# Kernel optimization log

Hardware: AMD Instinct MI355X
Metric: run time of the kernel (lower is better)

Reference implementation:

```python
import jax, jax.numpy as jnp
import numpy as np

B, S, D = 4, 4096, 2048
R_SSM = 6                      # ar_ssm_max_rank hardcoded in block
R_FFN = max(D // 96, 4)        # UltraLowRankFFN rank = 21
EPS = 1e-6


def rmsnorm(x, w):
    rms = jnp.sqrt(jnp.mean(x * x, axis=-1, keepdims=True) + EPS)
    return w * (x / rms)


def setup_inputs() -> dict:
    key = jax.random.key(0)
    ks = jax.random.split(key, 8)
    x = jax.random.normal(ks[0], (B, S, D), dtype=jnp.float32)
    norm1_w = jnp.ones((D,), dtype=jnp.float32)
    norm2_w = jnp.ones((D,), dtype=jnp.float32)
    # low-rank semiseparable AR-SSM params: in-proj U, decays lam, out-proj V
    U = jax.random.normal(ks[1], (D, R_SSM), dtype=jnp.float32) / np.sqrt(D)
    lam = jax.random.normal(ks[2], (R_SSM,), dtype=jnp.float32)
    V = jax.random.normal(ks[3], (R_SSM, D), dtype=jnp.float32) / np.sqrt(R_SSM)
    # ultra low-rank FFN
    W1 = jax.random.normal(ks[4], (D, R_FFN), dtype=jnp.float32) / np.sqrt(D)
    W2 = jax.random.normal(ks[5], (R_FFN, D), dtype=jnp.float32) / np.sqrt(R_FFN)
    return {"x": x, "norm1_w": norm1_w, "U": U, "lam": lam, "V": V,
            "norm2_w": norm2_w, "W1": W1, "W2": W2}


def reference(x, norm1_w, U, lam, V, norm2_w, W1, W2):
    # --- sublayer 1: RMSNorm -> low-rank semiseparable AR-SSM scan -> residual ---
    xn = rmsnorm(x, norm1_w)                     # [B,S,D]
    u = jnp.einsum('bsd,dr->bsr', xn, U)         # [B,S,r] low-rank input proj
    a = jax.nn.sigmoid(lam)                      # [r] stable decays in (0,1)

    def step(h, u_t):
        h = a * h + u_t                          # h: [B,r]
        return h, h

    h0 = jnp.zeros((B, R_SSM), dtype=x.dtype)
    _, hs = jax.lax.scan(step, h0, jnp.swapaxes(u, 0, 1))  # hs: [S,B,r]
    y = jnp.einsum('sbr,rd->bsd', hs, V)         # out proj back to d_model
    x = x + y

    # --- sublayer 2: RMSNorm -> ultra low-rank FFN (d->r->d, GELU) -> residual ---
    xn2 = rmsnorm(x, norm2_w)
    ffn = jnp.einsum('bsr,rd->bsd', jax.nn.gelu(jnp.einsum('bsd,dr->bsr', xn2, W1)), W2)
    return x + ffn
```

## Files before the change

kernel.cpp:

```cpp
#include <hip/hip_runtime.h>
#include <math.h>

namespace {
constexpr int S_ = 4096, D_ = 2048;
constexpr int RS_ = 6, RF_ = 21;
constexpr float EPS_ = 1e-6f;

typedef float floatx4 __attribute__((ext_vector_type(4)));

#define DPP_ADD_(v, ctrl) \
  v += __int_as_float(__builtin_amdgcn_update_dpp(0, __float_as_int(v), ctrl, 0xF, 0xF, true))

__device__ __forceinline__ float wave_sum(float v) {
  DPP_ADD_(v, 0x111);
  DPP_ADD_(v, 0x112);
  DPP_ADD_(v, 0x114);
  DPP_ADD_(v, 0x118);
  DPP_ADD_(v, 0x142);
  DPP_ADD_(v, 0x143);
  return __int_as_float(__builtin_amdgcn_readlane(__float_as_int(v), 63));
}

__device__ __forceinline__ float rdlane(float v, int l) {
  return __int_as_float(__builtin_amdgcn_readlane(__float_as_int(v), l));
}

__device__ __forceinline__ float sel_lane(float old, float val, int tgt, int lane) {
  return (lane == tgt) ? val : old;
}

__device__ __forceinline__ float gelu_f(float x) {
  float i2 = 1.5957691216057308f * fmaf(0.044715f * x * x, x, x);
  return x * __builtin_amdgcn_rcpf(1.f + __expf(-i2));
}

__device__ __forceinline__ float dot4(float4 a, float4 b) {
  return fmaf(a.x, b.x, fmaf(a.y, b.y, fmaf(a.z, b.z, a.w * b.w)));
}

__device__ __forceinline__ float4 fma4(float s, float4 a, float4 c) {
  return make_float4(fmaf(s, a.x, c.x), fmaf(s, a.y, c.y), fmaf(s, a.z, c.z),
                     fmaf(s, a.w, c.w));
}

__device__ __forceinline__ void ld4(float4 (&q)[4], const float* p) {
  q[0] = *(const float4*)(p);
  q[1] = *(const float4*)(p + 256);
  q[2] = *(const float4*)(p + 512);
  q[3] = *(const float4*)(p + 768);
}

__device__ __forceinline__ void nt_store4(float4 v, float* p) {
  floatx4 t = {v.x, v.y, v.z, v.w};
  __builtin_nontemporal_store(t, (floatx4*)p);
}
}

extern "C" __global__ void k_prep(const float* __restrict__ W1, const float* __restrict__ U,
                                  const float* __restrict__ n1w, const float* __restrict__ n2w,
                                  float* __restrict__ w1t, float* __restrict__ ut) {
  int t = blockIdx.x * 256 + threadIdx.x;
  if (t < D_ * RF_) {
    int d = t / RF_, j = t - d * RF_;
    w1t[j * D_ + d] = W1[t] * n2w[d];
  }
  int t2 = t - D_ * RF_;
  if (t2 >= 0 && t2 < D_ * RS_) {
    int d = t2 / RS_, r = t2 - d * RS_;
    ut[r * D_ + d] = U[t2] * n1w[d];
  }
}

extern "C" __global__ __launch_bounds__(256, 6) void k_rms1(
    const float* __restrict__ x, const float* __restrict__ ut,
    float* __restrict__ u_t) {
  int tid = threadIdx.x, lane = tid & 63, wid = tid >> 6;
  int row0 = blockIdx.x * 8 + wid * 2;
  int b = row0 >> 12;
  int sb = row0 & (S_ - 1);
  int d0 = lane * 4;
  const float* xr = x + (size_t)row0 * D_ + d0;
  const float* up = ut + d0;

  float s2a = 0.f, s2b = 0.f;
  float pa0 = 0.f, pa1 = 0.f, pa2 = 0.f, pa3 = 0.f, pa4 = 0.f, pa5 = 0.f;
  float pb0 = 0.f, pb1 = 0.f, pb2 = 0.f, pb3 = 0.f, pb4 = 0.f, pb5 = 0.f;
#pragma unroll
  for (int k = 0; k < 8; ++k) {
    float4 xa = *(const float4*)(xr + k * 256);
    float4 xb = *(const float4*)(xr + D_ + k * 256);
    s2a += dot4(xa, xa);
    s2b += dot4(xb, xb);
    float4 u0 = *(const float4*)(up + 0 * D_ + k * 256);
    pa0 += dot4(xa, u0); pb0 += dot4(xb, u0);
    float4 u1 = *(const float4*)(up + 1 * D_ + k * 256);
    pa1 += dot4(xa, u1); pb1 += dot4(xb, u1);
    float4 u2 = *(const float4*)(up + 2 * D_ + k * 256);
    pa2 += dot4(xa, u2); pb2 += dot4(xb, u2);
    float4 u3 = *(const float4*)(up + 3 * D_ + k * 256);
    pa3 += dot4(xa, u3); pb3 += dot4(xb, u3);
    float4 u4 = *(const float4*)(up + 4 * D_ + k * 256);
    pa4 += dot4(xa, u4); pb4 += dot4(xb, u4);
    float4 u5 = *(const float4*)(up + 5 * D_ + k * 256);
    pa5 += dot4(xa, u5); pb5 += dot4(xb, u5);
  }
  float ra = rsqrtf(wave_sum(s2a) * (1.0f / D_) + EPS_);
  float rb = rsqrtf(wave_sum(s2b) * (1.0f / D_) + EPS_);
  float va0 = wave_sum(pa0) * ra, vb0 = wave_sum(pb0) * rb;
  float va1 = wave_sum(pa1) * ra, vb1 = wave_sum(pb1) * rb;
  float va2 = wave_sum(pa2) * ra, vb2 = wave_sum(pb2) * rb;
  float va3 = wave_sum(pa3) * ra, vb3 = wave_sum(pb3) * rb;
  float va4 = wave_sum(pa4) * ra, vb4 = wave_sum(pb4) * rb;
  float va5 = wave_sum(pa5) * ra, vb5 = wave_sum(pb5) * rb;

  float uv = 0.f;
  uv = sel_lane(uv, va0, 0, lane);  uv = sel_lane(uv, vb0, 1, lane);
  uv = sel_lane(uv, va1, 2, lane);  uv = sel_lane(uv, vb1, 3, lane);
  uv = sel_lane(uv, va2, 4, lane);  uv = sel_lane(uv, vb2, 5, lane);
  uv = sel_lane(uv, va3, 6, lane);  uv = sel_lane(uv, vb3, 7, lane);
  uv = sel_lane(uv, va4, 8, lane);  uv = sel_lane(uv, vb4, 9, lane);
  uv = sel_lane(uv, va5, 10, lane); uv = sel_lane(uv, vb5, 11, lane);
  if (lane < 2 * RS_) {
    int r = lane >> 1, w = lane & 1;
    u_t[((size_t)b * RS_ + r) * S_ + sb + w] = uv;
  }
}

extern "C" __global__ __launch_bounds__(64) void k_scan(
    const float* __restrict__ lam, const float* __restrict__ u_t,
    float* __restrict__ hs_t) {
  int br = blockIdx.x;
  int r = br % RS_;
  int lane = threadIdx.x;
  float a = 1.f / (1.f + __expf(-lam[r]));
  float a64 = a;
#pragma unroll
  for (int i = 0; i < 6; ++i) a64 *= a64;

  const float* ub = u_t + (size_t)br * S_ + lane * 64;
  float vloc = 0.f;
#pragma unroll
  for (int i = 0; i < 16; ++i) {
    float4 uu = *(const float4*)(ub + i * 4);
    vloc = fmaf(a, vloc, uu.x);
    vloc = fmaf(a, vloc, uu.y);
    vloc = fmaf(a, vloc, uu.z);
    vloc = fmaf(a, vloc, uu.w);
  }
  float m = a64, v = vloc;
#pragma unroll
  for (int off = 1; off < 64; off <<= 1) {
    float mu = __shfl_up(m, off);
    float vu = __shfl_up(v, off);
    if (lane >= off) {
      v = fmaf(m, vu, v);
      m *= mu;
    }
  }
  float carry = __shfl_up(v, 1);
  if (lane == 0) carry = 0.f;

  float h = carry;
  float* hb = hs_t + (size_t)br * S_ + lane * 64;
#pragma unroll
  for (int i = 0; i < 16; ++i) {
    float4 uu = *(const float4*)(ub + i * 4);
    float4 o;
    h = fmaf(a, h, uu.x); o.x = h;
    h = fmaf(a, h, uu.y); o.y = h;
    h = fmaf(a, h, uu.z); o.z = h;
    h = fmaf(a, h, uu.w); o.w = h;
    *(float4*)(hb + i * 4) = o;
  }
}

#define DOT_HALF(Q, KB)                                           \
  {                                                               \
    p0 += dot4(xv[0][KB], Q[0]);   p0 += dot4(xv[0][KB+1], Q[1]); \
    p0 += dot4(xv[0][KB+2], Q[2]); p0 += dot4(xv[0][KB+3], Q[3]); \
    p1 += dot4(xv[1][KB], Q[0]);   p1 += dot4(xv[1][KB+1], Q[1]); \
    p1 += dot4(xv[1][KB+2], Q[2]); p1 += dot4(xv[1][KB+3], Q[3]); \
    p2 += dot4(xv[2][KB], Q[0]);   p2 += dot4(xv[2][KB+1], Q[1]); \
    p2 += dot4(xv[2][KB+2], Q[2]); p2 += dot4(xv[2][KB+3], Q[3]); \
    p3 += dot4(xv[3][KB], Q[0]);   p3 += dot4(xv[3][KB+1], Q[1]); \
    p3 += dot4(xv[3][KB+2], Q[2]); p3 += dot4(xv[3][KB+3], Q[3]); \
  }

#define FMA_HALF(Q, KB, F0, F1, F2, F3)                           \
  {                                                               \
    xv[0][KB]   = fma4(F0, Q[0], xv[0][KB]);                      \
    xv[0][KB+1] = fma4(F0, Q[1], xv[0][KB+1]);                    \
    xv[0][KB+2] = fma4(F0, Q[2], xv[0][KB+2]);                    \
    xv[0][KB+3] = fma4(F0, Q[3], xv[0][KB+3]);                    \
    xv[1][KB]   = fma4(F1, Q[0], xv[1][KB]);                      \
    xv[1][KB+1] = fma4(F1, Q[1], xv[1][KB+1]);                    \
    xv[1][KB+2] = fma4(F1, Q[2], xv[1][KB+2]);                    \
    xv[1][KB+3] = fma4(F1, Q[3], xv[1][KB+3]);                    \
    xv[2][KB]   = fma4(F2, Q[0], xv[2][KB]);                      \
    xv[2][KB+1] = fma4(F2, Q[1], xv[2][KB+1]);                    \
    xv[2][KB+2] = fma4(F2, Q[2], xv[2][KB+2]);                    \
    xv[2][KB+3] = fma4(F2, Q[3], xv[2][KB+3]);                    \
    xv[3][KB]   = fma4(F3, Q[0], xv[3][KB]);                      \
    xv[3][KB+1] = fma4(F3, Q[1], xv[3][KB+1]);                    \
    xv[3][KB+2] = fma4(F3, Q[2], xv[3][KB+2]);                    \
    xv[3][KB+3] = fma4(F3, Q[3], xv[3][KB+3]);                    \
  }

#define REDUCE_PACK(J)                                            \
  {                                                               \
    float t0 = wave_sum(p0) * rinv0;                              \
    float t1 = wave_sum(p1) * rinv1;                              \
    float t2 = wave_sum(p2) * rinv2;                              \
    float t3 = wave_sum(p3) * rinv3;                              \
    g0 = sel_lane(g0, t0, (J), lane);                             \
    g1 = sel_lane(g1, t1, (J), lane);                             \
    g2 = sel_lane(g2, t2, (J), lane);                             \
    g3 = sel_lane(g3, t3, (J), lane);                             \
  }

extern "C" __global__ __launch_bounds__(256, 2) void k_main(
    const float* __restrict__ x, const float* __restrict__ V,
    const float* __restrict__ w1t, const float* __restrict__ W2,
    const float* __restrict__ hs_t, float* __restrict__ out) {
  int tid = threadIdx.x, lane = tid & 63, wid = tid >> 6;
  int row0 = blockIdx.x * 16 + wid * 4;
  int b = row0 >> 12;
  int s0 = row0 & (S_ - 1);
  int d0 = lane * 4;

  float4 xv[4][8];
  const float* xr = x + (size_t)row0 * D_ + d0;
#pragma unroll
  for (int w = 0; w < 4; ++w)
#pragma unroll
    for (int k = 0; k < 8; ++k)
      xv[w][k] = *(const float4*)(xr + w * D_ + k * 256);

  float hv = 0.f;
  if (lane < 4 * RS_) {
    int w = lane / RS_, r = lane - w * RS_;
    hv = hs_t[((size_t)b * RS_ + r) * S_ + s0 + w];
  }

  float4 q0[4], q1[4], q2[4], q3[4];

  const float* Vp = V + d0;
  ld4(q0, Vp);
  ld4(q1, Vp + 1024);
  ld4(q2, Vp + D_);
#pragma unroll
  for (int rp = 0; rp < 3; ++rp) {
    int r0 = 2 * rp, r1 = 2 * rp + 1;
    ld4(q3, Vp + r1 * D_ + 1024);
    float h0 = rdlane(hv, 0 * RS_ + r0), h1 = rdlane(hv, 1 * RS_ + r0);
    float h2 = rdlane(hv, 2 * RS_ + r0), h3 = rdlane(hv, 3 * RS_ + r0);
    FMA_HALF(q0, 0, h0, h1, h2, h3);
    if (rp < 2) ld4(q0, Vp + (r0 + 2) * D_);
    FMA_HALF(q1, 4, h0, h1, h2, h3);
    if (rp < 2) ld4(q1, Vp + (r1 + 1) * D_ + 1024);
    float e0 = rdlane(hv, 0 * RS_ + r1), e1 = rdlane(hv, 1 * RS_ + r1);
    float e2 = rdlane(hv, 2 * RS_ + r1), e3 = rdlane(hv, 3 * RS_ + r1);
    FMA_HALF(q2, 0, e0, e1, e2, e3);
    if (rp < 2) ld4(q2, Vp + (r1 + 2) * D_);
    FMA_HALF(q3, 4, e0, e1, e2, e3);
  }

  const float* Wp = w1t + d0;
  ld4(q0, Wp);
  ld4(q1, Wp + 1024);
  ld4(q2, Wp + D_);

  float s20 = 0.f, s21 = 0.f, s22 = 0.f, s23 = 0.f;
#pragma unroll
  for (int k = 0; k < 8; ++k) {
    s20 += dot4(xv[0][k], xv[0][k]);
    s21 += dot4(xv[1][k], xv[1][k]);
    s22 += dot4(xv[2][k], xv[2][k]);
    s23 += dot4(xv[3][k], xv[3][k]);
  }
  float rinv0 = rsqrtf(wave_sum(s20) * (1.0f / D_) + EPS_);
  float rinv1 = rsqrtf(wave_sum(s21) * (1.0f / D_) + EPS_);
  float rinv2 = rsqrtf(wave_sum(s22) * (1.0f / D_) + EPS_);
  float rinv3 = rsqrtf(wave_sum(s23) * (1.0f / D_) + EPS_);

  float g0 = 0.f, g1 = 0.f, g2 = 0.f, g3 = 0.f;
  float p0, p1, p2, p3;
  for (int jp = 0; jp < 10; ++jp) {
    int j0 = 2 * jp, j1 = 2 * jp + 1;
    ld4(q3, Wp + j1 * D_ + 1024);
    p0 = p1 = p2 = p3 = 0.f;
    DOT_HALF(q0, 0);
    ld4(q0, Wp + (j0 + 2) * D_);
    DOT_HALF(q1, 4);
    REDUCE_PACK(j0);
    ld4(q1, Wp + (j1 + 1) * D_ + 1024);
    p0 = p1 = p2 = p3 = 0.f;
    DOT_HALF(q2, 0);
    if (jp < 9) ld4(q2, Wp + (j1 + 2) * D_);
    DOT_HALF(q3, 4);
    REDUCE_PACK(j1);
  }
  p0 = p1 = p2 = p3 = 0.f;
  DOT_HALF(q0, 0);
  DOT_HALF(q1, 4);
  const float* W2p = W2 + d0;
  REDUCE_PACK(20);
  ld4(q0, W2p);
  ld4(q1, W2p + 1024);
  ld4(q2, W2p + D_);
  g0 = gelu_f(g0); g1 = gelu_f(g1); g2 = gelu_f(g2); g3 = gelu_f(g3);

  for (int jp = 0; jp < 10; ++jp) {
    int j0 = 2 * jp, j1 = 2 * jp + 1;
    ld4(q3, W2p + j1 * D_ + 1024);
    float f0 = rdlane(g0, j0), f1 = rdlane(g1, j0);
    float f2 = rdlane(g2, j0), f3 = rdlane(g3, j0);
    FMA_HALF(q0, 0, f0, f1, f2, f3);
    ld4(q0, W2p + (j0 + 2) * D_);
    FMA_HALF(q1, 4, f0, f1, f2, f3);
    ld4(q1, W2p + (j1 + 1) * D_ + 1024);
    float e0 = rdlane(g0, j1), e1 = rdlane(g1, j1);
    float e2 = rdlane(g2, j1), e3 = rdlane(g3, j1);
    FMA_HALF(q2, 0, e0, e1, e2, e3);
    if (jp < 9) ld4(q2, W2p + (j1 + 2) * D_);
    FMA_HALF(q3, 4, e0, e1, e2, e3);
  }
  {
    float f0 = rdlane(g0, 20), f1 = rdlane(g1, 20);
    float f2 = rdlane(g2, 20), f3 = rdlane(g3, 20);
    FMA_HALF(q0, 0, f0, f1, f2, f3);
    FMA_HALF(q1, 4, f0, f1, f2, f3);
  }

  float* orow = out + (size_t)row0 * D_ + d0;
#pragma unroll
  for (int w = 0; w < 4; ++w)
#pragma unroll
    for (int k = 0; k < 8; ++k)
      nt_store4(xv[w][k], orow + w * D_ + k * 256);
}

extern "C" void kernel_launch(void* const* d_in, const int* in_sizes, int n_in,
                              void* d_out, int out_size, void* d_ws, size_t ws_size,
                              hipStream_t stream) {
  const float* x   = (const float*)d_in[0];
  const float* n1w = (const float*)d_in[1];
  const float* U   = (const float*)d_in[2];
  const float* lam = (const float*)d_in[3];
  const float* V   = (const float*)d_in[4];
  const float* n2w = (const float*)d_in[5];
  const float* W1  = (const float*)d_in[6];
  const float* W2  = (const float*)d_in[7];
  float* out = (float*)d_out;
  float* ws  = (float*)d_ws;

  float* u_t  = ws;
  float* hs_t = ws + 98304;
  float* w1t  = ws + 196608;
  float* ut   = ws + 239616;

  k_prep<<<216, 256, 0, stream>>>(W1, U, n1w, n2w, w1t, ut);
  k_rms1<<<2048, 256, 0, stream>>>(x, ut, u_t);
  k_scan<<<24, 64, 0, stream>>>(lam, u_t, hs_t);
  k_main<<<1024, 256, 0, stream>>>(x, V, w1t, W2, hs_t, out);
}
```

Before: 332.8 us.

## Compute FFN down-projection with bf16 MFMA via LDS-staged normalized activations

Replaces the per-row fp32 dot products and wave reductions for the D->21 projection with bf16 MFMA 16x16x32. Normalized rows are packed to bf16 into a padded LDS tile, W1 is pre-swizzled into MFMA operand layout in k_prep, and each wave handles a K-slice with partial sums reduced through shared memory before GELU. This is meant to remove the many DPP wave_sum reductions and the scalar FMA work, at the cost of about 70KB of LDS per block (which limits occupancy), extra barriers, and bf16 rounding error in the first FFN projection.

```diff
diff --git a/kernel.cpp b/kernel.cpp
--- a/kernel.cpp
+++ b/kernel.cpp
@@ -7,6 +7,7 @@
 constexpr float EPS_ = 1e-6f;
 
 typedef float floatx4 __attribute__((ext_vector_type(4)));
+typedef short bf16x8 __attribute__((ext_vector_type(8)));
 
 #define DPP_ADD_(v, ctrl) \
   v += __int_as_float(__builtin_amdgcn_update_dpp(0, __float_as_int(v), ctrl, 0xF, 0xF, true))
@@ -25,10 +26,6 @@
   return __int_as_float(__builtin_amdgcn_readlane(__float_as_int(v), l));
 }
 
-__device__ __forceinline__ float sel_lane(float old, float val, int tgt, int lane) {
-  return (lane == tgt) ? val : old;
-}
-
 __device__ __forceinline__ float gelu_f(float x) {
   float i2 = 1.5957691216057308f * fmaf(0.044715f * x * x, x, x);
   return x * __builtin_amdgcn_rcpf(1.f + __expf(-i2));
@@ -54,20 +51,33 @@
   floatx4 t = {v.x, v.y, v.z, v.w};
   __builtin_nontemporal_store(t, (floatx4*)p);
 }
+
+__device__ __forceinline__ unsigned int bf16_bits(float f) {
+  unsigned int u = __float_as_uint(f);
+  return (u + 0x7fffu + ((u >> 16) & 1u)) >> 16;
+}
+__device__ __forceinline__ unsigned int pack_bf16(float a, float b) {
+  return bf16_bits(a) | (bf16_bits(b) << 16);
+}
 }
 
 extern "C" __global__ void k_prep(const float* __restrict__ W1, const float* __restrict__ U,
                                   const float* __restrict__ n1w, const float* __restrict__ n2w,
-                                  float* __restrict__ w1t, float* __restrict__ ut) {
+                                  unsigned short* __restrict__ w1f, float* __restrict__ ut) {
   int t = blockIdx.x * 256 + threadIdx.x;
-  if (t < D_ * RF_) {
-    int d = t / RF_, j = t - d * RF_;
-    w1t[j * D_ + d] = W1[t] * n2w[d];
-  }
-  int t2 = t - D_ * RF_;
-  if (t2 >= 0 && t2 < D_ * RS_) {
-    int d = t2 / RS_, r = t2 - d * RS_;
-    ut[r * D_ + d] = U[t2] * n1w[d];
+  if (t < 65536) {
+    int i = t & 7, lane = (t >> 3) & 63, ntk = t >> 9;
+    int nt = ntk & 1, kt = ntk >> 1;
+    int k = kt * 32 + ((lane >> 4) << 3) + i;
+    int j = nt * 16 + (lane & 15);
+    float v = (j < RF_) ? W1[k * RF_ + j] * n2w[k] : 0.f;
+    w1f[t] = (unsigned short)bf16_bits(v);
+  } else {
+    int t2 = t - 65536;
+    if (t2 < D_ * RS_) {
+      int d = t2 / RS_, r = t2 - d * RS_;
+      ut[r * D_ + d] = U[t2] * n1w[d];
+    }
   }
 }
 
@@ -114,12 +124,12 @@
   float va5 = wave_sum(pa5) * ra, vb5 = wave_sum(pb5) * rb;
 
   float uv = 0.f;
-  uv = sel_lane(uv, va0, 0, lane);  uv = sel_lane(uv, vb0, 1, lane);
-  uv = sel_lane(uv, va1, 2, lane);  uv = sel_lane(uv, vb1, 3, lane);
-  uv = sel_lane(uv, va2, 4, lane);  uv = sel_lane(uv, vb2, 5, lane);
-  uv = sel_lane(uv, va3, 6, lane);  uv = sel_lane(uv, vb3, 7, lane);
-  uv = sel_lane(uv, va4, 8, lane);  uv = sel_lane(uv, vb4, 9, lane);
-  uv = sel_lane(uv, va5, 10, lane); uv = sel_lane(uv, vb5, 11, lane);
+  uv = (lane == 0) ? va0 : uv;  uv = (lane == 1) ? vb0 : uv;
+  uv = (lane == 2) ? va1 : uv;  uv = (lane == 3) ? vb1 : uv;
+  uv = (lane == 4) ? va2 : uv;  uv = (lane == 5) ? vb2 : uv;
+  uv = (lane == 6) ? va3 : uv;  uv = (lane == 7) ? vb3 : uv;
+  uv = (lane == 8) ? va4 : uv;  uv = (lane == 9) ? vb4 : uv;
+  uv = (lane == 10) ? va5 : uv; uv = (lane == 11) ? vb5 : uv;
   if (lane < 2 * RS_) {
     int r = lane >> 1, w = lane & 1;
     u_t[((size_t)b * RS_ + r) * S_ + sb + w] = uv;
@@ -173,18 +183,6 @@
     *(float4*)(hb + i * 4) = o;
   }
 }
-
-#define DOT_HALF(Q, KB)                                           \
-  {                                                               \
-    p0 += dot4(xv[0][KB], Q[0]);   p0 += dot4(xv[0][KB+1], Q[1]); \
-    p0 += dot4(xv[0][KB+2], Q[2]); p0 += dot4(xv[0][KB+3], Q[3]); \
-    p1 += dot4(xv[1][KB], Q[0]);   p1 += dot4(xv[1][KB+1], Q[1]); \
-    p1 += dot4(xv[1][KB+2], Q[2]); p1 += dot4(xv[1][KB+3], Q[3]); \
-    p2 += dot4(xv[2][KB], Q[0]);   p2 += dot4(xv[2][KB+1], Q[1]); \
-    p2 += dot4(xv[2][KB+2], Q[2]); p2 += dot4(xv[2][KB+3], Q[3]); \
-    p3 += dot4(xv[3][KB], Q[0]);   p3 += dot4(xv[3][KB+1], Q[1]); \
-    p3 += dot4(xv[3][KB+2], Q[2]); p3 += dot4(xv[3][KB+3], Q[3]); \
-  }
 
 #define FMA_HALF(Q, KB, F0, F1, F2, F3)                           \
   {                                                               \
@@ -206,22 +204,28 @@
     xv[3][KB+3] = fma4(F3, Q[3], xv[3][KB+3]);                    \
   }
 
-#define REDUCE_PACK(J)                                            \
-  {                                                               \
-    float t0 = wave_sum(p0) * rinv0;                              \
-    float t1 = wave_sum(p1) * rinv1;                              \
-    float t2 = wave_sum(p2) * rinv2;                              \
-    float t3 = wave_sum(p3) * rinv3;                              \
-    g0 = sel_lane(g0, t0, (J), lane);                             \
-    g1 = sel_lane(g1, t1, (J), lane);                             \
-    g2 = sel_lane(g2, t2, (J), lane);                             \
-    g3 = sel_lane(g3, t3, (J), lane);                             \
+#define STAGE(W, RW)                                                        \
+  {                                                                         \
+    int row_ = wid * 4 + (W);                                               \
+    _Pragma("unroll") for (int c = 0; c < 8; ++c) {                         \
+      int d_ = lane * 4 + c * 256;                                          \
+      unsigned int lo_ = pack_bf16(xv[W][c].x * (RW), xv[W][c].y * (RW));   \
+      unsigned int hi_ = pack_bf16(xv[W][c].z * (RW), xv[W][c].w * (RW));   \
+      int raw_ = ((d_ >> 5) << 10) | (((d_ >> 3) & 3) << 8) |               \
+                 (row_ << 4) | ((d_ & 7) << 1);                             \
+      int pad_ = raw_ + ((raw_ >> 8) << 4);                                 \
+      *(uint2*)(abuf + pad_) = make_uint2(lo_, hi_);                        \
+    }                                                                       \
   }
 
 extern "C" __global__ __launch_bounds__(256, 2) void k_main(
     const float* __restrict__ x, const float* __restrict__ V,
-    const float* __restrict__ w1t, const float* __restrict__ W2,
+    const unsigned short* __restrict__ w1f, const float* __restrict__ W2,
     const float* __restrict__ hs_t, float* __restrict__ out) {
+  __shared__ __align__(16) unsigned char abuf[69632];
+  __shared__ float cpart[8][256];
+  __shared__ float tbuf[16][24];
+
   int tid = threadIdx.x, lane = tid & 63, wid = tid >> 6;
   int row0 = blockIdx.x * 16 + wid * 4;
   int b = row0 >> 12;
@@ -265,11 +269,6 @@
     FMA_HALF(q3, 4, e0, e1, e2, e3);
   }
 
-  const float* Wp = w1t + d0;
-  ld4(q0, Wp);
-  ld4(q1, Wp + 1024);
-  ld4(q2, Wp + D_);
-
   float s20 = 0.f, s21 = 0.f, s22 = 0.f, s23 = 0.f;
 #pragma unroll
   for (int k = 0; k < 8; ++k) {
@@ -283,33 +282,57 @@
   float rinv2 = rsqrtf(wave_sum(s22) * (1.0f / D_) + EPS_);
   float rinv3 = rsqrtf(wave_sum(s23) * (1.0f / D_) + EPS_);
 
-  float g0 = 0.f, g1 = 0.f, g2 = 0.f, g3 = 0.f;
-  float p0, p1, p2, p3;
-  for (int jp = 0; jp < 10; ++jp) {
-    int j0 = 2 * jp, j1 = 2 * jp + 1;
-    ld4(q3, Wp + j1 * D_ + 1024);
-    p0 = p1 = p2 = p3 = 0.f;
-    DOT_HALF(q0, 0);
-    ld4(q0, Wp + (j0 + 2) * D_);
-    DOT_HALF(q1, 4);
-    REDUCE_PACK(j0);
-    ld4(q1, Wp + (j1 + 1) * D_ + 1024);
-    p0 = p1 = p2 = p3 = 0.f;
-    DOT_HALF(q2, 0);
-    if (jp < 9) ld4(q2, Wp + (j1 + 2) * D_);
-    DOT_HALF(q3, 4);
-    REDUCE_PACK(j1);
-  }
-  p0 = p1 = p2 = p3 = 0.f;
-  DOT_HALF(q0, 0);
-  DOT_HALF(q1, 4);
+  STAGE(0, rinv0);
+  STAGE(1, rinv1);
+  STAGE(2, rinv2);
+  STAGE(3, rinv3);
+  __syncthreads();
+
+  {
+    floatx4 acc0 = {0.f, 0.f, 0.f, 0.f};
+    floatx4 acc1 = {0.f, 0.f, 0.f, 0.f};
+#pragma unroll 4
+    for (int t = 0; t < 16; ++t) {
+      int kt = wid * 16 + t;
+      int raw = (kt << 10) | ((lane >> 4) << 8) | ((lane & 15) << 4);
+      int pad = raw + ((raw >> 8) << 4);
+      bf16x8 a = *(const bf16x8*)(abuf + pad);
+      bf16x8 b0 = *(const bf16x8*)(w1f + (size_t)(kt * 2 + 0) * 512 + lane * 8);
+      bf16x8 b1 = *(const bf16x8*)(w1f + (size_t)(kt * 2 + 1) * 512 + lane * 8);
+      acc0 = __builtin_amdgcn_mfma_f32_16x16x32_bf16(a, b0, acc0, 0, 0, 0);
+      acc1 = __builtin_amdgcn_mfma_f32_16x16x32_bf16(a, b1, acc1, 0, 0, 0);
+    }
+    *(floatx4*)&cpart[wid * 2 + 0][lane * 4] = acc0;
+    *(floatx4*)&cpart[wid * 2 + 1][lane * 4] = acc1;
+  }
+  __syncthreads();
+
+  if (tid < 128) {
+    int nt = tid >> 6, pos = tid & 63;
+    floatx4 s = *(const floatx4*)&cpart[nt][pos * 4];
+    s += *(const floatx4*)&cpart[2 + nt][pos * 4];
+    s += *(const floatx4*)&cpart[4 + nt][pos * 4];
+    s += *(const floatx4*)&cpart[6 + nt][pos * 4];
+    int col = pos & 15, rg = pos >> 4;
+    int j = nt * 16 + col;
+    if (j < RF_) {
+      tbuf[rg * 4 + 0][j] = gelu_f(s.x);
+      tbuf[rg * 4 + 1][j] = gelu_f(s.y);
+      tbuf[rg * 4 + 2][j] = gelu_f(s.z);
+      tbuf[rg * 4 + 3][j] = gelu_f(s.w);
+    }
+  }
+  __syncthreads();
+
+  float g0 = (lane < RF_) ? tbuf[wid * 4 + 0][lane] : 0.f;
+  float g1 = (lane < RF_) ? tbuf[wid * 4 + 1][lane] : 0.f;
+  float g2 = (lane < RF_) ? tbuf[wid * 4 + 2][lane] : 0.f;
+  float g3 = (lane < RF_) ? tbuf[wid * 4 + 3][lane] : 0.f;
+
   const float* W2p = W2 + d0;
-  REDUCE_PACK(20);
   ld4(q0, W2p);
   ld4(q1, W2p + 1024);
   ld4(q2, W2p + D_);
-  g0 = gelu_f(g0); g1 = gelu_f(g1); g2 = gelu_f(g2); g3 = gelu_f(g3);
-
   for (int jp = 0; jp < 10; ++jp) {
     int j0 = 2 * jp, j1 = 2 * jp + 1;
     ld4(q3, W2p + j1 * D_ + 1024);
@@ -354,13 +377,13 @@
   float* out = (float*)d_out;
   float* ws  = (float*)d_ws;
 
-  float* u_t  = ws;
+  float* u_t = ws;
   float* hs_t = ws + 98304;
-  float* w1t  = ws + 196608;
-  float* ut   = ws + 239616;
-
-  k_prep<<<216, 256, 0, stream>>>(W1, U, n1w, n2w, w1t, ut);
+  unsigned short* w1f = (unsigned short*)(ws + 196608);
+  float* ut = ws + 229376;
+
+  k_prep<<<304, 256, 0, stream>>>(W1, U, n1w, n2w, w1f, ut);
   k_rms1<<<2048, 256, 0, stream>>>(x, ut, u_t);
   k_scan<<<24, 64, 0, stream>>>(lam, u_t, hs_t);
-  k_main<<<1024, 256, 0, stream>>>(x, V, w1t, W2, hs_t, out);
-}
+  k_main<<<1024, 256, 0, stream>>>(x, V, w1f, W2, hs_t, out);
+}
```

After: 327.3 us. No clear change (-1.6%).
